# Performance work log

Hardware: AMD Instinct MI355X
Metric: run time of the kernel (lower is better)

## Reference

```python
import jax, jax.numpy as jnp
import numpy as np

B, NS, NW, L, DL, DS, OUT, VOCAB = 32, 8, 32, 196, 1024, 2048, 512, 3266
SCALE = 0.05


def setup_inputs() -> dict:
    key = jax.random.key(0)
    ks = jax.random.split(key, 15)
    r = lambda k, shape: jax.random.normal(k, shape, dtype=jnp.float32)
    return {
        "local_features": r(ks[0], (B, DL, L)),
        "sentenc": r(ks[1], (B, NS, DS)),
        "W_s": r(ks[2], (L, DS)) * SCALE,
        "W_v": r(ks[3], (L, DL)) * SCALE,
        "W_a": r(ks[4], (1, L)) * SCALE,
        "W_ih1": r(ks[5], (4 * OUT, DL)) * SCALE,
        "W_hh1": r(ks[6], (4 * OUT, OUT)) * SCALE,
        "b_ih1": r(ks[7], (4 * OUT,)) * SCALE,
        "b_hh1": r(ks[8], (4 * OUT,)) * SCALE,
        "W_ih2": r(ks[9], (4 * OUT, OUT)) * SCALE,
        "W_hh2": r(ks[10], (4 * OUT, OUT)) * SCALE,
        "b_ih2": r(ks[11], (4 * OUT,)) * SCALE,
        "b_hh2": r(ks[12], (4 * OUT,)) * SCALE,
        "W_f": r(ks[13], (VOCAB, OUT)) * SCALE,
        "b_f": r(ks[14], (VOCAB,)) * SCALE,
    }


def _lstm_cell(x, h, c, W_ih, W_hh, b_ih, b_hh):
    # PyTorch LSTMCell: gates order i, f, g, o
    gates = x @ W_ih.T + b_ih + h @ W_hh.T + b_hh
    i, f, g, o = jnp.split(gates, 4, axis=-1)
    c_new = jax.nn.sigmoid(f) * c + jax.nn.sigmoid(i) * jnp.tanh(g)
    h_new = jax.nn.sigmoid(o) * jnp.tanh(c_new)
    return h_new, c_new


def reference(local_features, sentenc, W_s, W_v, W_a,
              W_ih1, W_hh1, b_ih1, b_hh1,
              W_ih2, W_hh2, b_ih2, b_hh2, W_f, b_f):
    # ---- additive (Bahdanau-style) attention, vectorized over sentences ----
    sent = jnp.einsum('bns,ls->bnl', sentenc, W_s)           # [B,NS,L]
    vis = jnp.einsum('bdi,ld->bil', local_features, W_v)     # [B,L(loc i),L(out l)]
    tot = jnp.tanh(vis[:, None, :, :] + sent[:, :, :, None]) # [B,NS,L,L]
    a = jnp.einsum('bnil,l->bni', tot, W_a[0])                # [B,NS,L]
    # original code: softmax over a size-1 trailing dim -> all-ones weights
    a_soft = jax.nn.softmax(a[..., None], axis=-1)[..., 0]    # [B,NS,L], == 1.0
    final = jnp.einsum('bni,bdi->bnd', a_soft, local_features)  # [B,NS,DL]

    # ---- dual-LSTMCell decoder: same attended input repeated NW times ----
    xs = jnp.broadcast_to(final[:, :, None, :], (B, NS, NW, DL))
    xs = xs.reshape(B, NS * NW, DL).transpose(1, 0, 2)        # [T,B,DL]

    def step(carry, x):
        h, c, h1, c1 = carry
        h, c = _lstm_cell(x, h, c, W_ih1, W_hh1, b_ih1, b_hh1)
        h1, c1 = _lstm_cell(h, h1, c1, W_ih2, W_hh2, b_ih2, b_hh2)
        word = h1 @ W_f.T + b_f
        return (h, c, h1, c1), word

    z = jnp.zeros((B, OUT), dtype=local_features.dtype)
    _, words = jax.lax.scan(step, (z, z, z, z), xs)           # [T,B,VOCAB]
    word_list = words.reshape(NS, NW, B, VOCAB).transpose(2, 0, 1, 3)
    return word_list
```

## Files before the change

### kernel.cpp

```cpp
#include <hip/hip_runtime.h>
#include <hip/hip_bf16.h>

#define B_     32
#define DL_    1024
#define L_     196
#define OUT_   512
#define G4_    2048
#define T_     256
#define VOCAB_ 3266
#define NWG_L1  32
#define NWG_L2  64
#define NWG_REC (NWG_L1 + NWG_L2)
#define NSL_    8

#define SIG_STRIDE_ (NSL_ * 16)
#define SIG_BYTES_  (257 * SIG_STRIDE_ * 4)
#define OFF_SH   0
#define OFF_SH1  (SIG_BYTES_)
#define OFF_SR2  (2 * SIG_BYTES_)
#define OFF_X    (3 * SIG_BYTES_)
#define OFF_XW1  (OFF_X + B_*DL_*4)
#define OFF_B2   (OFF_XW1 + B_*G4_*4)
#define OFF_HP   (OFF_B2 + G4_*4)
#define OFF_H1   (OFF_HP + 4*B_*OUT_*2)

typedef _Float16 half8 __attribute__((ext_vector_type(8)));
typedef float floatx4 __attribute__((ext_vector_type(4)));

__device__ __forceinline__ float sigmf(float v) { return 1.0f / (1.0f + __expf(-v)); }

__device__ __forceinline__ unsigned short f2h(float f) {
  union { _Float16 h; unsigned short u; } c;
  c.h = (_Float16)f;
  return c.u;
}

__device__ __forceinline__ half8 ldw8(const float* p) {
  float4 q0 = *(const float4*)p;
  float4 q1 = *(const float4*)(p + 4);
  half8 r;
  r[0] = (_Float16)q0.x; r[1] = (_Float16)q0.y; r[2] = (_Float16)q0.z; r[3] = (_Float16)q0.w;
  r[4] = (_Float16)q1.x; r[5] = (_Float16)q1.y; r[6] = (_Float16)q1.z; r[7] = (_Float16)q1.w;
  return r;
}

__device__ __forceinline__ half8 pack8(float4 a, float4 b) {
  half8 r;
  r[0] = (_Float16)a.x; r[1] = (_Float16)a.y; r[2] = (_Float16)a.z; r[3] = (_Float16)a.w;
  r[4] = (_Float16)b.x; r[5] = (_Float16)b.y; r[6] = (_Float16)b.z; r[7] = (_Float16)b.w;
  return r;
}

__device__ __forceinline__ unsigned long long ld8(const unsigned long long* p) {
  return __hip_atomic_load(p, __ATOMIC_RELAXED, __HIP_MEMORY_SCOPE_AGENT);
}
__device__ __forceinline__ void st8(unsigned long long* p, unsigned long long v) {
  __hip_atomic_store(p, v, __ATOMIC_RELAXED, __HIP_MEMORY_SCOPE_AGENT);
}

__device__ __forceinline__ void sigadd(unsigned int* arr, int q, int wg) {
  __hip_atomic_fetch_add(&arr[q * SIG_STRIDE_ + (wg & (NSL_ - 1)) * 16], 1u,
                         __ATOMIC_RELAXED, __HIP_MEMORY_SCOPE_AGENT);
}

__device__ __forceinline__ void pollge(unsigned int* p, unsigned tgt, unsigned* dead) {
  if (*dead) return;
  unsigned polls = 0;
  while (__hip_atomic_load(p, __ATOMIC_RELAXED, __HIP_MEMORY_SCOPE_AGENT) < tgt) {
    __builtin_amdgcn_s_sleep(2);
    if (++polls > 400000u) { *dead = 1; break; }
  }
}

__global__ __launch_bounds__(256) void k_rowsum(const float* __restrict__ lf, float* __restrict__ x) {
  int t = blockIdx.x * 256 + threadIdx.x;
  const float4* p = (const float4*)(lf + (size_t)t * L_);
  float s = 0.f;
  #pragma unroll
  for (int i = 0; i < 49; ++i) { float4 v = p[i]; s += (v.x + v.y) + (v.z + v.w); }
  x[t] = s;
}

__global__ __launch_bounds__(256) void k_xw1(const float* __restrict__ x, const float* __restrict__ Wih1,
                                             const float* __restrict__ bih1, const float* __restrict__ bhh1,
                                             const float* __restrict__ bih2, const float* __restrict__ bhh2,
                                             float* __restrict__ xw1, float* __restrict__ bias2) {
  int t = blockIdx.x * 256 + threadIdx.x;
  int b = t >> 11, j = t & (G4_ - 1);
  const float4* xp = (const float4*)(x + (size_t)b * DL_);
  const float4* wp = (const float4*)(Wih1 + (size_t)j * DL_);
  float s = 0.f;
  #pragma unroll 8
  for (int i = 0; i < DL_ / 4; ++i) {
    float4 a = xp[i], w = wp[i];
    s += a.x * w.x + a.y * w.y + a.z * w.z + a.w * w.w;
  }
  xw1[t] = s + bih1[j] + bhh1[j];
  if (t < G4_) bias2[t] = bih2[t] + bhh2[t];
}

__global__ __launch_bounds__(256, 1) void k_rec(const float* __restrict__ Whh1,
                                                const float* __restrict__ Wih2,
                                                const float* __restrict__ Whh2,
                                                const float* __restrict__ xw1,
                                                const float* __restrict__ bias2,
                                                unsigned short* __restrict__ Hp,
                                                unsigned short* __restrict__ H1,
                                                unsigned int* __restrict__ sh,
                                                unsigned int* __restrict__ sh1,
                                                unsigned int* __restrict__ sr2) {
  __shared__ __align__(16) unsigned short sm[16896];
  unsigned long long* smu = (unsigned long long*)sm;
  const int wg = blockIdx.x, tid = threadIdx.x;
  unsigned dead = 0;
  unsigned long long* Hpu = (unsigned long long*)Hp;
  unsigned long long* H1u = (unsigned long long*)H1;
  const int wv = tid >> 6, l = tid & 63, lr = l & 15, kg = l >> 4;
  const int swz = lr & 7;

  if (wg < NWG_L1) {
    const int u0 = (wg * 4 + wv) * 4;
    half8 wf[16];
    {
      const int j = (lr & 3) * 512 + u0 + (lr >> 2);
      const float* wr = Whh1 + (size_t)j * OUT_ + kg * 8;
      #pragma unroll
      for (int kt = 0; kt < 16; ++kt) wf[kt] = ldw8(wr + kt * 32);
    }
    floatx4 xb0, xb1;
    #pragma unroll
    for (int g = 0; g < 4; ++g) {
      xb0[g] = xw1[lr * G4_ + g * OUT_ + u0 + kg];
      xb1[g] = xw1[(16 + lr) * G4_ + g * OUT_ + u0 + kg];
    }
    float cs0 = 0.f, cs1 = 0.f;

    for (int q = 0; q < T_; ++q) {
      if (q > 0) {
        if (tid < 8) pollge(&sh[q * SIG_STRIDE_ + tid * 16], 4, &dead);
        else if (tid >= 16 && tid < 24 && q >= 4)
          pollge(&sr2[(q - 3) * SIG_STRIDE_ + (tid - 16) * 16], 8, &dead);
        __syncthreads();
      }
      const unsigned long long* src = Hpu + (size_t)(q & 3) * 4096;
      unsigned long long v[16];
      #pragma unroll
      for (int i = 0; i < 16; ++i) v[i] = ld8(src + i * 256 + tid);
      #pragma unroll
      for (int i = 0; i < 16; ++i) {
        int w = i * 256 + tid;
        int b = w >> 7, c8 = w & 127, k8 = c8 >> 1, hf = c8 & 1;
        smu[b * 128 + ((k8 ^ (b & 7)) << 1) + hf] = v[i];
      }
      __syncthreads();

      floatx4 a0 = xb0, a1 = xb1;
      #pragma unroll
      for (int kt = 0; kt < 16; ++kt) {
        int c0 = ((kt * 4 + kg) ^ swz) * 8;
        half8 h0 = *(const half8*)&sm[lr * 512 + c0];
        half8 h1 = *(const half8*)&sm[(16 + lr) * 512 + c0];
        a0 = __builtin_amdgcn_mfma_f32_16x16x32_f16(wf[kt], h0, a0, 0, 0, 0);
        a1 = __builtin_amdgcn_mfma_f32_16x16x32_f16(wf[kt], h1, a1, 0, 0, 0);
      }
      {
        float i0 = sigmf(a0[0]), f0 = sigmf(a0[1]), g0 = tanhf(a0[2]), o0 = sigmf(a0[3]);
        cs0 = fmaf(f0, cs0, i0 * g0);
        float hv0 = o0 * tanhf(cs0);
        float i1 = sigmf(a1[0]), f1 = sigmf(a1[1]), g1 = tanhf(a1[2]), o1 = sigmf(a1[3]);
        cs1 = fmaf(f1, cs1, i1 * g1);
        float hv1 = o1 * tanhf(cs1);
        sm[16384 + lr * 16 + wv * 4 + kg] = f2h(hv0);
        sm[16384 + (16 + lr) * 16 + wv * 4 + kg] = f2h(hv1);
      }
      __syncthreads();
      if (tid < 128) {
        int b = tid >> 2, uw = tid & 3;
        st8(Hpu + (size_t)((q + 1) & 3) * 4096 + (size_t)b * 128 + wg * 4 + uw,
            smu[4096 + b * 4 + uw]);
      }
      __syncthreads();
      if (tid == 0) sigadd(sh, q + 1, wg);
    }
  } else {
    const int wl = wg - NWG_L1;
    const int ub = wl >> 1;
    const int b0 = (wl & 1) * 16;
    const int u0 = (ub * 4 + wv) * 4;
    half8 wf[32];
    {
      const int j = (lr & 3) * 512 + u0 + (lr >> 2);
      const float* wi = Wih2 + (size_t)j * OUT_ + kg * 8;
      const float* wh = Whh2 + (size_t)j * OUT_ + kg * 8;
      #pragma unroll
      for (int kt = 0; kt < 16; ++kt) wf[kt] = ldw8(wi + kt * 32);
      #pragma unroll
      for (int kt = 0; kt < 16; ++kt) wf[16 + kt] = ldw8(wh + kt * 32);
    }
    floatx4 bs;
    #pragma unroll
    for (int g = 0; g < 4; ++g) bs[g] = bias2[g * OUT_ + u0 + kg];
    float cs = 0.f;

    for (int q = 1; q <= T_; ++q) {
      if (tid < 8) pollge(&sh[q * SIG_STRIDE_ + tid * 16], 4, &dead);
      else if (tid >= 8 && tid < 16 && q >= 2)
        pollge(&sh1[(q - 1) * SIG_STRIDE_ + (tid - 8) * 16], 8, &dead);
      __syncthreads();

      const unsigned long long* shp  = Hpu + (size_t)(q & 3) * 4096;
      const unsigned long long* sh1p = H1u + (size_t)(q - 1) * 4096;
      unsigned long long v[16];
      #pragma unroll
      for (int i = 0; i < 16; ++i) {
        int w = i * 256 + tid;
        int row = w >> 8, c8 = w & 255, k8 = c8 >> 1, hf = c8 & 1;
        v[i] = (k8 < 64) ? ld8(shp  + (size_t)(b0 + row) * 128 + (k8 << 1) + hf)
                         : ld8(sh1p + (size_t)(b0 + row) * 128 + ((k8 - 64) << 1) + hf);
      }
      #pragma unroll
      for (int i = 0; i < 16; ++i) {
        int w = i * 256 + tid;
        int row = w >> 8, c8 = w & 255, k8 = c8 >> 1, hf = c8 & 1;
        smu[row * 256 + ((k8 ^ (row & 7)) << 1) + hf] = v[i];
      }
      __syncthreads();
      if (tid == 0) sigadd(sr2, q, wg);

      floatx4 a0 = bs;
      #pragma unroll
      for (int kt = 0; kt < 32; ++kt) {
        int c0 = ((kt * 4 + kg) ^ swz) * 8;
        half8 xv = *(const half8*)&sm[lr * 1024 + c0];
        a0 = __builtin_amdgcn_mfma_f32_16x16x32_f16(wf[kt], xv, a0, 0, 0, 0);
      }
      {
        float i0 = sigmf(a0[0]), f0 = sigmf(a0[1]), g0 = tanhf(a0[2]), o0 = sigmf(a0[3]);
        cs = fmaf(f0, cs, i0 * g0);
        float h1v = o0 * tanhf(cs);
        sm[16384 + lr * 16 + wv * 4 + kg] = f2h(h1v);
      }
      __syncthreads();
      if (tid < 64) {
        int row = tid >> 2, uw = tid & 3;
        st8(H1u + (size_t)q * 4096 + (size_t)(b0 + row) * 128 + ub * 4 + uw,
            smu[4096 + row * 4 + uw]);
      }
      __syncthreads();
      if (tid == 0) sigadd(sh1, q, wg);
    }
  }
}

__global__ __launch_bounds__(256, 2) void k_gemm(const unsigned short* __restrict__ H1,
                                                 const float* __restrict__ Wf,
                                                 const float* __restrict__ bfv,
                                                 float* __restrict__ out) {
  __shared__ __align__(16) unsigned short Asm[128 * 56];
  __shared__ __align__(16) unsigned short Bsm[128 * 56];
  const int mt = blockIdx.x, nt = blockIdx.y, tid = threadIdx.x;
  const int wv = tid >> 6, l = tid & 63, lr = l & 15, kg = l >> 4;
  floatx4 acc[2][8];
  #pragma unroll
  for (int m = 0; m < 2; ++m)
    #pragma unroll
    for (int n = 0; n < 8; ++n) acc[m][n] = (floatx4){0.f, 0.f, 0.f, 0.f};

  const unsigned short* Abase = H1 + (size_t)(32 + mt * 128) * OUT_;
  const int r = tid >> 1, kh = (tid & 1) * 16;
  const int vr = nt * 128 + r;

  for (int k0 = 0; k0 < OUT_; k0 += 32) {
    {
      const uint4* srcA = (const uint4*)(Abase + (size_t)r * OUT_ + k0 + kh);
      uint4 a0 = srcA[0], a1 = srcA[1];
      *(uint4*)&Asm[r * 56 + kh]     = a0;
      *(uint4*)&Asm[r * 56 + kh + 8] = a1;
    }
    {
      float4 f0 = {0,0,0,0}, f1 = f0, f2 = f0, f3 = f0;
      if (vr < VOCAB_) {
        const float4* wsrc = (const float4*)(Wf + (size_t)vr * OUT_ + k0 + kh);
        f0 = wsrc[0]; f1 = wsrc[1]; f2 = wsrc[2]; f3 = wsrc[3];
      }
      *(half8*)&Bsm[r * 56 + kh]     = pack8(f0, f1);
      *(half8*)&Bsm[r * 56 + kh + 8] = pack8(f2, f3);
    }
    __syncthreads();

    const int co = kg * 8;
    half8 a0f = *(const half8*)&Asm[(wv * 32 + lr) * 56 + co];
    half8 a1f = *(const half8*)&Asm[(wv * 32 + 16 + lr) * 56 + co];
    #pragma unroll
    for (int n = 0; n < 8; ++n) {
      half8 bf = *(const half8*)&Bsm[(n * 16 + lr) * 56 + co];
      acc[0][n] = __builtin_amdgcn_mfma_f32_16x16x32_f16(a0f, bf, acc[0][n], 0, 0, 0);
      acc[1][n] = __builtin_amdgcn_mfma_f32_16x16x32_f16(a1f, bf, acc[1][n], 0, 0, 0);
    }
    __syncthreads();
  }

  #pragma unroll
  for (int n = 0; n < 8; ++n) {
    int vcol = nt * 128 + n * 16 + lr;
    if (vcol >= VOCAB_) continue;
    float bias = bfv[vcol];
    #pragma unroll
    for (int m = 0; m < 2; ++m)
      #pragma unroll
      for (int g = 0; g < 4; ++g) {
        int mg = mt * 128 + wv * 32 + m * 16 + kg * 4 + g;
        int bb = mg & 31, s = mg >> 5;
        out[(size_t)(bb * 256 + s) * VOCAB_ + vcol] = acc[m][n][g] + bias;
      }
  }
}

extern "C" void kernel_launch(void* const* d_in, const int* in_sizes, int n_in,
                              void* d_out, int out_size, void* d_ws, size_t ws_size,
                              hipStream_t stream) {
  const float* lf   = (const float*)d_in[0];
  const float* Wih1 = (const float*)d_in[5];
  const float* Whh1 = (const float*)d_in[6];
  const float* bih1 = (const float*)d_in[7];
  const float* bhh1 = (const float*)d_in[8];
  const float* Wih2 = (const float*)d_in[9];
  const float* Whh2 = (const float*)d_in[10];
  const float* bih2 = (const float*)d_in[11];
  const float* bhh2 = (const float*)d_in[12];
  const float* Wf   = (const float*)d_in[13];
  const float* bfv  = (const float*)d_in[14];
  float* out = (float*)d_out;
  char* ws = (char*)d_ws;

  unsigned int*   sh   = (unsigned int*)(ws + OFF_SH);
  unsigned int*   sh1  = (unsigned int*)(ws + OFF_SH1);
  unsigned int*   sr2  = (unsigned int*)(ws + OFF_SR2);
  float*          x    = (float*)(ws + OFF_X);
  float*          xw1  = (float*)(ws + OFF_XW1);
  float*          b2   = (float*)(ws + OFF_B2);
  unsigned short* Hp   = (unsigned short*)(ws + OFF_HP);
  unsigned short* H1   = (unsigned short*)(ws + OFF_H1);

  (void)hipMemsetAsync(ws, 0, 3 * SIG_BYTES_, stream);
  (void)hipMemsetAsync(Hp, 0, 4 * B_ * OUT_ * 2, stream);
  (void)hipMemsetAsync(H1, 0, B_ * OUT_ * 2, stream);

  k_rowsum<<<128, 256, 0, stream>>>(lf, x);
  k_xw1<<<256, 256, 0, stream>>>(x, Wih1, bih1, bhh1, bih2, bhh2, xw1, b2);

  void* kargs[] = {(void*)&Whh1, (void*)&Wih2, (void*)&Whh2, (void*)&xw1, (void*)&b2,
                   (void*)&Hp, (void*)&H1, (void*)&sh, (void*)&sh1, (void*)&sr2};
  hipError_t cerr = hipLaunchCooperativeKernel((void*)k_rec, dim3(NWG_REC), dim3(256),
                                               kargs, 0, stream);
  if (cerr != hipSuccess) {
    k_rec<<<NWG_REC, 256, 0, stream>>>(Whh1, Wih2, Whh2, xw1, b2, Hp, H1, sh, sh1, sr2);
  }

  k_gemm<<<dim3(64, 26), 256, 0, stream>>>(H1, Wf, bfv, out);
}
```

Baseline: 1.211 ms.

## Halve layer-1 workgroups, deepen h ring buffer, split layer-2 signals per batch half

Layer-1 recurrent workgroups drop from 32 to 16, and each now computes 8 hidden units with two weight fragment sets and four MFMA accumulators. This cuts the number of producers each step must wait for. The Hp ring buffer grows from 4 to 8 slots, so layer 1 can run up to 7 steps ahead of layer 2 before waiting on its reads. The layer-2 completion counters are split per batch half, so each layer-2 group waits only for the 32 groups producing its own rows. In exchange, each layer-1 group does twice the MFMA and activation work per step and holds more registers, which lengthens the serial critical path of layer 1.

```diff
diff --git a/kernel.cpp b/kernel.cpp
--- a/kernel.cpp
+++ b/kernel.cpp
@@ -8,21 +8,21 @@
 #define G4_    2048
 #define T_     256
 #define VOCAB_ 3266
-#define NWG_L1  32
+#define NWG_L1  16
 #define NWG_L2  64
 #define NWG_REC (NWG_L1 + NWG_L2)
 #define NSL_    8
 
 #define SIG_STRIDE_ (NSL_ * 16)
-#define SIG_BYTES_  (257 * SIG_STRIDE_ * 4)
+#define SIG_Q_      (257 * SIG_STRIDE_ * 4)
 #define OFF_SH   0
-#define OFF_SH1  (SIG_BYTES_)
-#define OFF_SR2  (2 * SIG_BYTES_)
-#define OFF_X    (3 * SIG_BYTES_)
+#define OFF_SH1  (SIG_Q_)
+#define OFF_SR2  (OFF_SH1 + 2 * SIG_Q_)
+#define OFF_X    (OFF_SR2 + SIG_Q_)
 #define OFF_XW1  (OFF_X + B_*DL_*4)
 #define OFF_B2   (OFF_XW1 + B_*G4_*4)
 #define OFF_HP   (OFF_B2 + G4_*4)
-#define OFF_H1   (OFF_HP + 4*B_*OUT_*2)
+#define OFF_H1   (OFF_HP + 8*B_*OUT_*2)
 
 typedef _Float16 half8 __attribute__((ext_vector_type(8)));
 typedef float floatx4 __attribute__((ext_vector_type(4)));
@@ -58,9 +58,8 @@
   __hip_atomic_store(p, v, __ATOMIC_RELAXED, __HIP_MEMORY_SCOPE_AGENT);
 }
 
-__device__ __forceinline__ void sigadd(unsigned int* arr, int q, int wg) {
-  __hip_atomic_fetch_add(&arr[q * SIG_STRIDE_ + (wg & (NSL_ - 1)) * 16], 1u,
-                         __ATOMIC_RELAXED, __HIP_MEMORY_SCOPE_AGENT);
+__device__ __forceinline__ void sigraw(unsigned int* p) {
+  __hip_atomic_fetch_add(p, 1u, __ATOMIC_RELAXED, __HIP_MEMORY_SCOPE_AGENT);
 }
 
 __device__ __forceinline__ void pollge(unsigned int* p, unsigned tgt, unsigned* dead) {
@@ -109,7 +108,7 @@
                                                 unsigned int* __restrict__ sh,
                                                 unsigned int* __restrict__ sh1,
                                                 unsigned int* __restrict__ sr2) {
-  __shared__ __align__(16) unsigned short sm[16896];
+  __shared__ __align__(16) unsigned short sm[17408];
   unsigned long long* smu = (unsigned long long*)sm;
   const int wg = blockIdx.x, tid = threadIdx.x;
   unsigned dead = 0;
@@ -119,30 +118,34 @@
   const int swz = lr & 7;
 
   if (wg < NWG_L1) {
-    const int u0 = (wg * 4 + wv) * 4;
-    half8 wf[16];
+    const int u0 = (wg * 4 + wv) * 8;
+    half8 wfa[16], wfb[16];
     {
-      const int j = (lr & 3) * 512 + u0 + (lr >> 2);
-      const float* wr = Whh1 + (size_t)j * OUT_ + kg * 8;
-      #pragma unroll
-      for (int kt = 0; kt < 16; ++kt) wf[kt] = ldw8(wr + kt * 32);
-    }
-    floatx4 xb0, xb1;
+      const int ja = (lr & 3) * 512 + u0 + (lr >> 2);
+      const int jb = (lr & 3) * 512 + (u0 + 4) + (lr >> 2);
+      const float* wra = Whh1 + (size_t)ja * OUT_ + kg * 8;
+      const float* wrb = Whh1 + (size_t)jb * OUT_ + kg * 8;
+      #pragma unroll
+      for (int kt = 0; kt < 16; ++kt) { wfa[kt] = ldw8(wra + kt * 32); wfb[kt] = ldw8(wrb + kt * 32); }
+    }
+    floatx4 xb00, xb01, xb10, xb11;
     #pragma unroll
     for (int g = 0; g < 4; ++g) {
-      xb0[g] = xw1[lr * G4_ + g * OUT_ + u0 + kg];
-      xb1[g] = xw1[(16 + lr) * G4_ + g * OUT_ + u0 + kg];
-    }
-    float cs0 = 0.f, cs1 = 0.f;
+      xb00[g] = xw1[lr * G4_ + g * OUT_ + u0 + kg];
+      xb01[g] = xw1[(16 + lr) * G4_ + g * OUT_ + u0 + kg];
+      xb10[g] = xw1[lr * G4_ + g * OUT_ + u0 + 4 + kg];
+      xb11[g] = xw1[(16 + lr) * G4_ + g * OUT_ + u0 + 4 + kg];
+    }
+    float cs00 = 0.f, cs01 = 0.f, cs10 = 0.f, cs11 = 0.f;
 
     for (int q = 0; q < T_; ++q) {
       if (q > 0) {
-        if (tid < 8) pollge(&sh[q * SIG_STRIDE_ + tid * 16], 4, &dead);
-        else if (tid >= 16 && tid < 24 && q >= 4)
-          pollge(&sr2[(q - 3) * SIG_STRIDE_ + (tid - 16) * 16], 8, &dead);
+        if (tid < 8) pollge(&sh[q * SIG_STRIDE_ + tid * 16], 2, &dead);
+        else if (tid >= 16 && tid < 24 && q >= 8)
+          pollge(&sr2[(q - 7) * SIG_STRIDE_ + (tid - 16) * 16], 8, &dead);
         __syncthreads();
       }
-      const unsigned long long* src = Hpu + (size_t)(q & 3) * 4096;
+      const unsigned long long* src = Hpu + (size_t)(q & 7) * 4096;
       unsigned long long v[16];
       #pragma unroll
       for (int i = 0; i < 16; ++i) v[i] = ld8(src + i * 256 + tid);
@@ -154,39 +157,48 @@
       }
       __syncthreads();
 
-      floatx4 a0 = xb0, a1 = xb1;
+      floatx4 a00 = xb00, a01 = xb01, a10 = xb10, a11 = xb11;
       #pragma unroll
       for (int kt = 0; kt < 16; ++kt) {
         int c0 = ((kt * 4 + kg) ^ swz) * 8;
         half8 h0 = *(const half8*)&sm[lr * 512 + c0];
         half8 h1 = *(const half8*)&sm[(16 + lr) * 512 + c0];
-        a0 = __builtin_amdgcn_mfma_f32_16x16x32_f16(wf[kt], h0, a0, 0, 0, 0);
-        a1 = __builtin_amdgcn_mfma_f32_16x16x32_f16(wf[kt], h1, a1, 0, 0, 0);
+        a00 = __builtin_amdgcn_mfma_f32_16x16x32_f16(wfa[kt], h0, a00, 0, 0, 0);
+        a01 = __builtin_amdgcn_mfma_f32_16x16x32_f16(wfa[kt], h1, a01, 0, 0, 0);
+        a10 = __builtin_amdgcn_mfma_f32_16x16x32_f16(wfb[kt], h0, a10, 0, 0, 0);
+        a11 = __builtin_amdgcn_mfma_f32_16x16x32_f16(wfb[kt], h1, a11, 0, 0, 0);
       }
       {
-        float i0 = sigmf(a0[0]), f0 = sigmf(a0[1]), g0 = tanhf(a0[2]), o0 = sigmf(a0[3]);
-        cs0 = fmaf(f0, cs0, i0 * g0);
-        float hv0 = o0 * tanhf(cs0);
-        float i1 = sigmf(a1[0]), f1 = sigmf(a1[1]), g1 = tanhf(a1[2]), o1 = sigmf(a1[3]);
-        cs1 = fmaf(f1, cs1, i1 * g1);
-        float hv1 = o1 * tanhf(cs1);
-        sm[16384 + lr * 16 + wv * 4 + kg] = f2h(hv0);
-        sm[16384 + (16 + lr) * 16 + wv * 4 + kg] = f2h(hv1);
-      }
-      __syncthreads();
-      if (tid < 128) {
-        int b = tid >> 2, uw = tid & 3;
-        st8(Hpu + (size_t)((q + 1) & 3) * 4096 + (size_t)b * 128 + wg * 4 + uw,
-            smu[4096 + b * 4 + uw]);
-      }
-      __syncthreads();
-      if (tid == 0) sigadd(sh, q + 1, wg);
+        float i0, f0, g0, o0;
+        i0 = sigmf(a00[0]); f0 = sigmf(a00[1]); g0 = tanhf(a00[2]); o0 = sigmf(a00[3]);
+        cs00 = fmaf(f0, cs00, i0 * g0);
+        sm[16384 + lr * 32 + wv * 8 + kg] = f2h(o0 * tanhf(cs00));
+        i0 = sigmf(a01[0]); f0 = sigmf(a01[1]); g0 = tanhf(a01[2]); o0 = sigmf(a01[3]);
+        cs01 = fmaf(f0, cs01, i0 * g0);
+        sm[16384 + (16 + lr) * 32 + wv * 8 + kg] = f2h(o0 * tanhf(cs01));
+        i0 = sigmf(a10[0]); f0 = sigmf(a10[1]); g0 = tanhf(a10[2]); o0 = sigmf(a10[3]);
+        cs10 = fmaf(f0, cs10, i0 * g0);
+        sm[16384 + lr * 32 + wv * 8 + 4 + kg] = f2h(o0 * tanhf(cs10));
+        i0 = sigmf(a11[0]); f0 = sigmf(a11[1]); g0 = tanhf(a11[2]); o0 = sigmf(a11[3]);
+        cs11 = fmaf(f0, cs11, i0 * g0);
+        sm[16384 + (16 + lr) * 32 + wv * 8 + 4 + kg] = f2h(o0 * tanhf(cs11));
+      }
+      __syncthreads();
+      {
+        int row = tid >> 3, chunk = tid & 7;
+        st8(Hpu + (size_t)((q + 1) & 7) * 4096 + (size_t)row * 128 + wg * 8 + chunk,
+            smu[4096 + row * 8 + chunk]);
+      }
+      __syncthreads();
+      if (tid == 0) sigraw(&sh[(q + 1) * SIG_STRIDE_ + (wg & 7) * 16]);
     }
   } else {
     const int wl = wg - NWG_L1;
+    const int half = wl & 1;
     const int ub = wl >> 1;
-    const int b0 = (wl & 1) * 16;
+    const int b0 = half * 16;
     const int u0 = (ub * 4 + wv) * 4;
+    const int slot2 = (wl >> 1) & 7;
     half8 wf[32];
     {
       const int j = (lr & 3) * 512 + u0 + (lr >> 2);
@@ -203,12 +215,12 @@
     float cs = 0.f;
 
     for (int q = 1; q <= T_; ++q) {
-      if (tid < 8) pollge(&sh[q * SIG_STRIDE_ + tid * 16], 4, &dead);
+      if (tid < 8) pollge(&sh[q * SIG_STRIDE_ + tid * 16], 2, &dead);
       else if (tid >= 8 && tid < 16 && q >= 2)
-        pollge(&sh1[(q - 1) * SIG_STRIDE_ + (tid - 8) * 16], 8, &dead);
-      __syncthreads();
-
-      const unsigned long long* shp  = Hpu + (size_t)(q & 3) * 4096;
+        pollge(&sh1[(q - 1) * 2 * SIG_STRIDE_ + half * SIG_STRIDE_ + (tid - 8) * 16], 4, &dead);
+      __syncthreads();
+
+      const unsigned long long* shp  = Hpu + (size_t)(q & 7) * 4096;
       const unsigned long long* sh1p = H1u + (size_t)(q - 1) * 4096;
       unsigned long long v[16];
       #pragma unroll
@@ -225,7 +237,7 @@
         smu[row * 256 + ((k8 ^ (row & 7)) << 1) + hf] = v[i];
       }
       __syncthreads();
-      if (tid == 0) sigadd(sr2, q, wg);
+      if (tid == 0) sigraw(&sr2[q * SIG_STRIDE_ + (wg & 7) * 16]);
 
       floatx4 a0 = bs;
       #pragma unroll
@@ -247,7 +259,7 @@
             smu[4096 + row * 4 + uw]);
       }
       __syncthreads();
-      if (tid == 0) sigadd(sh1, q, wg);
+      if (tid == 0) sigraw(&sh1[q * 2 * SIG_STRIDE_ + half * SIG_STRIDE_ + slot2 * 16]);
     }
   }
 }
@@ -342,8 +354,8 @@
   unsigned short* Hp   = (unsigned short*)(ws + OFF_HP);
   unsigned short* H1   = (unsigned short*)(ws + OFF_H1);
 
-  (void)hipMemsetAsync(ws, 0, 3 * SIG_BYTES_, stream);
-  (void)hipMemsetAsync(Hp, 0, 4 * B_ * OUT_ * 2, stream);
+  (void)hipMemsetAsync(ws, 0, OFF_X, stream);
+  (void)hipMemsetAsync(Hp, 0, 8 * B_ * OUT_ * 2, stream);
   (void)hipMemsetAsync(H1, 0, B_ * OUT_ * 2, stream);
 
   k_rowsum<<<128, 256, 0, stream>>>(lf, x);
```

Measured after the change: 1.164 ms (median of 2 runs). 3.9% less time.
